# Kernel tuning notes

Measured on AMD Instinct MI355X. Metric: run time of the kernel, lower is better.

The kernel has to match this reference:

```python
import jax, jax.numpy as jnp
import numpy as np

CHAN = 24
INNER = 64
GROUPS = 8
M = 5
LAM = 1e-4
MAX_ITER = 25
BETA = 1.0
EPS = 1e-5
B, HH, WW = 128, 32, 32


def conv2d(x, w, b=None):
    # NCHW, OIHW, 3x3 SAME conv (padding = kernel//2)
    y = jax.lax.conv_general_dilated(x, w, (1, 1), 'SAME',
                                     dimension_numbers=('NCHW', 'OIHW', 'NCHW'))
    if b is not None:
        y = y + b[None, :, None, None]
    return y


def group_norm(x, g, b):
    bsz, c, h, w = x.shape
    xg = x.reshape(bsz, GROUPS, c // GROUPS, h, w)
    mu = xg.mean(axis=(2, 3, 4), keepdims=True)
    var = xg.var(axis=(2, 3, 4), keepdims=True)
    xn = ((xg - mu) / jnp.sqrt(var + EPS)).reshape(bsz, c, h, w)
    return xn * g[None, :, None, None] + b[None, :, None, None]


def batch_norm(x, g, b):
    # training-mode batch statistics over (N, H, W)
    mu = x.mean(axis=(0, 2, 3), keepdims=True)
    var = x.var(axis=(0, 2, 3), keepdims=True)
    return (x - mu) / jnp.sqrt(var + EPS) * g[None, :, None, None] + b[None, :, None, None]


def resnet_f(p, z, x):
    c1w, g1g, g1b, c2w, g2g, g2b, g3g, g3b = p
    y = group_norm(jax.nn.relu(conv2d(z, c1w)), g1g, g1b)
    return group_norm(jax.nn.relu(z + group_norm(x + conv2d(y, c2w), g2g, g2b)), g3g, g3b)


def anderson(f, x0):
    # Anderson acceleration, fixed MAX_ITER iterations (no host-sync tol break).
    bsz = x0.shape[0]
    d = x0.size // bsz
    X = jnp.zeros((bsz, M, d), x0.dtype)
    Fm = jnp.zeros((bsz, M, d), x0.dtype)
    f0 = f(x0).reshape(bsz, -1)
    X = X.at[:, 0].set(x0.reshape(bsz, -1))
    Fm = Fm.at[:, 0].set(f0)
    X = X.at[:, 1].set(f0)
    Fm = Fm.at[:, 1].set(f(f0.reshape(x0.shape)).reshape(bsz, -1))
    for k in range(2, MAX_ITER):
        n = min(k, M)
        G = Fm[:, :n] - X[:, :n]                       # [b, n, d]
        Hm = jnp.zeros((bsz, n + 1, n + 1), x0.dtype)
        Hm = Hm.at[:, 0, 1:].set(1.0).at[:, 1:, 0].set(1.0)
        Hm = Hm.at[:, 1:, 1:].set(jnp.einsum('bnd,bmd->bnm', G, G)
                                  + LAM * jnp.eye(n, dtype=x0.dtype)[None])
        yv = jnp.zeros((bsz, n + 1, 1), x0.dtype).at[:, 0, 0].set(1.0)
        alpha = jnp.linalg.solve(Hm, yv)[:, 1:, 0]     # [b, n]
        xnew = (BETA * jnp.einsum('bn,bnd->bd', alpha, Fm[:, :n])
                + (1.0 - BETA) * jnp.einsum('bn,bnd->bd', alpha, X[:, :n]))
        X = X.at[:, k % M].set(xnew)
        Fm = Fm.at[:, k % M].set(f(xnew.reshape(x0.shape)).reshape(bsz, -1))
    return X[:, (MAX_ITER - 1) % M].reshape(x0.shape)


def setup_inputs() -> dict:
    key = jax.random.key(0)
    ks = jax.random.split(key, 8)
    inp = {
        'x': jax.random.normal(ks[0], (B, 3, HH, WW), jnp.float32),
        'pre_conv_w': jax.random.normal(ks[1], (CHAN, 3, 3, 3), jnp.float32) * 0.1,
        'pre_conv_b': jnp.zeros((CHAN,), jnp.float32),
        'pre_bn_g': jnp.ones((CHAN,), jnp.float32),
        'pre_bn_b': jnp.zeros((CHAN,), jnp.float32),
        'f_conv1_w': jax.random.normal(ks[2], (INNER, CHAN, 3, 3), jnp.float32) * 0.01,
        'gn1_g': jnp.ones((INNER,), jnp.float32),
        'gn1_b': jnp.zeros((INNER,), jnp.float32),
        'f_conv2_w': jax.random.normal(ks[3], (CHAN, INNER, 3, 3), jnp.float32) * 0.01,
        'gn2_g': jnp.ones((CHAN,), jnp.float32),
        'gn2_b': jnp.zeros((CHAN,), jnp.float32),
        'gn3_g': jnp.ones((CHAN,), jnp.float32),
        'gn3_b': jnp.zeros((CHAN,), jnp.float32),
        'post_bn_g': jnp.ones((CHAN,), jnp.float32),
        'post_bn_b': jnp.zeros((CHAN,), jnp.float32),
        'fc_w': jax.random.normal(ks[4], (10, CHAN * 4 * 4), jnp.float32) * 0.05,
        'fc_b': jnp.zeros((10,), jnp.float32),
    }
    return inp


def reference(x, pre_conv_w, pre_conv_b, pre_bn_g, pre_bn_b,
              f_conv1_w, gn1_g, gn1_b, f_conv2_w, gn2_g, gn2_b, gn3_g, gn3_b,
              post_bn_g, post_bn_b, fc_w, fc_b):
    # pre: conv + BatchNorm
    xp = batch_norm(conv2d(x, pre_conv_w, pre_conv_b), pre_bn_g, pre_bn_b)
    p = (f_conv1_w, gn1_g, gn1_b, f_conv2_w, gn2_g, gn2_b, gn3_g, gn3_b)
    # DEQ fixed-point solve (eval path: train=False returns the fixed point)
    z_star = anderson(lambda z: resnet_f(p, z, xp), jnp.zeros_like(xp))
    z = resnet_f(p, z_star, xp)
    # post: relu -> BN -> avgpool(8,8) -> flatten -> linear
    h = batch_norm(jax.nn.relu(z), post_bn_g, post_bn_b)
    bsz, c, hh, ww = h.shape
    pooled = h.reshape(bsz, c, hh // 8, 8, ww // 8, 8).mean(axis=(3, 5))  # [B,C,4,4]
    return pooled.reshape(bsz, -1) @ fc_w.T + fc_b
```

## Files before the change

kernel.cpp:

```cpp
#include <hip/hip_runtime.h>
#include <hip/hip_bf16.h>

typedef __hip_bfloat16 bf16;
typedef unsigned short ushortT;
typedef __attribute__((ext_vector_type(8))) short short8;
typedef __attribute__((ext_vector_type(4))) float f32x4;

#define BB 128
#define CHAN 24
#define INNER 64
#define HW 1024
#define DD (CHAN*HW)

constexpr size_t cBD = (size_t)BB*DD;
constexpr size_t cYB = (size_t)BB*INNER*HW;

__device__ __attribute__((aligned(16))) ushortT g_xp[cBD];
__device__ __attribute__((aligned(16))) ushortT g_X[5*cBD];
__device__ __attribute__((aligned(16))) ushortT g_F[5*cBD];
__device__ __attribute__((aligned(16))) ushortT g_G[5*cBD];
__device__ __attribute__((aligned(16))) ushortT g_yb[cYB];
__device__ __attribute__((aligned(16))) ushortT g_tb[cBD];
__device__ __attribute__((aligned(16))) ushortT g_w1m[9*64*32];
__device__ __attribute__((aligned(16))) ushortT g_w2m[9*24*64];
__device__ __attribute__((aligned(16))) float g_stats2a[48];
__device__ __attribute__((aligned(16))) float g_stats2b[48];
__device__ __attribute__((aligned(16))) float g_gn1sum[BB*8*2];
__device__ __attribute__((aligned(16))) float g_gn2sum[BB*24*2];
__device__ __attribute__((aligned(16))) float g_gn3p[BB*4*16];
__device__ __attribute__((aligned(16))) float g_gramp[BB*4*5*5];
__device__ __attribute__((aligned(16))) float g_gram[BB*25];
__device__ __attribute__((aligned(16))) float g_pooled[BB*CHAN*16];
__device__ __attribute__((aligned(16))) float g_params[5120];
__device__ unsigned g_isbf16;

#define P_PCW 0
#define P_PCB 648
#define P_PBG 672
#define P_PBB 696
#define P_G1G 720
#define P_G1B 784
#define P_G2G 848
#define P_G2B 872
#define P_G3G 896
#define P_G3B 920
#define P_POG 944
#define P_POB 968
#define P_FCW 992
#define P_FCB 4832

__device__ __forceinline__ size_t aidx(int b, int icv, int pix){
  return (((size_t)b*3 + icv)*1024 + (size_t)pix)*8;
}
__device__ __forceinline__ float rdin(const void* p, int i){
// ... 50 lines not shown
                              g_params[P_POG+i]=rdin(pog,i);
                              g_params[P_POB+i]=rdin(pob,i); }
  for (int i=t;i<64;i+=256) { g_params[P_G1G+i]=rdin(g1g,i);
                              g_params[P_G1B+i]=rdin(g1b,i); }
  for (int i=t;i<3840;i+=256) g_params[P_FCW+i]=rdin(fcw,i);
  for (int i=t;i<10;i+=256)   g_params[P_FCB+i]=rdin(fcb,i);
  for (int i=t;i<48;i+=256) { g_stats2a[i]=0.f; g_stats2b[i]=0.f; }
}

__global__ void wtm_k(const void* w1, const void* w2){
  int t = blockIdx.x*256 + threadIdx.x;
  if (t < 9*64*32){
    int ic = t & 31, oc = (t>>5)&63, s9 = t>>11;
    float v = (ic<24) ? rdin(w1, (oc*24+ic)*9 + s9) : 0.f;
    g_w1m[t] = f2b(v);
  }
  int u = t - 9*64*32;
  if (u >= 0 && u < 9*24*64){
    int ic = u & 63; int rest = u >> 6; int oc = rest % 24; int s9 = rest / 24;
    g_w2m[u] = f2b(rdin(w2, (oc*64+ic)*9 + s9));
  }
}

__global__ void zeroX0_k(){
  size_t i = ((size_t)blockIdx.x*256 + threadIdx.x)*8;
  short8 z = {0,0,0,0,0,0,0,0};
  *(short8*)&g_X[i] = z;
  if (blockIdx.x < 8) g_gn1sum[blockIdx.x*256 + threadIdx.x] = 0.f;
}
__global__ void copyF0toX1_k(){
  size_t i = ((size_t)blockIdx.x*256 + threadIdx.x)*8;
  *(short8*)&g_X[cBD + i] = *(const short8*)&g_F[i];
  if (blockIdx.x < 8) g_gn1sum[blockIdx.x*256 + threadIdx.x] = 0.f;
}

__global__ void preconv_k(const void* __restrict__ x){
  int id = blockIdx.x*256 + threadIdx.x;
  int b = id >> 10, pix = id & 1023;
  int yy = pix >> 5, xx = pix & 31;
  float acc[24];
  #pragma unroll
  for (int oc=0;oc<24;oc++) acc[oc] = g_params[P_PCB+oc];
  for (int ic=0; ic<3; ic++)
    for (int ky=0; ky<3; ky++){
      int gy = yy+ky-1; if (gy<0||gy>=32) continue;
      for (int kx=0;kx<3;kx++){
        int gx = xx+kx-1; if (gx<0||gx>=32) continue;
        float v = rdin(x, ((b*3+ic)*32+gy)*32+gx);
        #pragma unroll
        for (int oc=0;oc<24;oc++)
          acc[oc] += v * g_params[P_PCW+(oc*3+ic)*9+ky*3+kx];
      }
    }
  st24c(g_tb, b, pix, acc);
}

template<bool RELU>
__global__ void bnstat2_k(int which){
// ... 22 lines not shown
    atomicAdd(&sRed[(icv*8+e)*2],   p0[e]);
    atomicAdd(&sRed[(icv*8+e)*2+1], p1[e]);
  }
  __syncthreads();
  if (t < 48) atomicAdd(&dst[t], sRed[t]);
}

__global__ void bn_apply_k(){
  int id = blockIdx.x*256+threadIdx.x;
  int b = id >> 10, pix = id & 1023;
  const float inv = 1.f/(BB*HW);
  float tv[24], ov[24];
  ld24c(g_tb, b, pix, tv);
  #pragma unroll
  for (int c=0;c<24;c++){
    float mean = g_stats2a[c*2]*inv;
    float var = fmaxf(g_stats2a[c*2+1]*inv - mean*mean, 0.f);
    float rstd = rsqrtf(var + 1e-5f);
    ov[c] = (tv[c]-mean)*rstd*g_params[P_PBG+c] + g_params[P_PBB+c];
  }
  st24c(g_xp, b, pix, ov);
}

__launch_bounds__(256, 2)
__global__ void conv1_k(int s){
  __shared__ ushortT sMem[29312];
  ushortT* sA = sMem;
  ushortT* sW = sMem + 10880;
  const int tid = threadIdx.x;
  const int lane = tid & 63, wv = tid >> 6;
  const int mLane = lane & 15, q = lane >> 4;
  const int b = blockIdx.x >> 2, yt = blockIdx.x & 3;
  const ushortT* __restrict__ Xs = g_X + (size_t)s*cBD;
  if (blockIdx.x < 24) g_gn2sum[blockIdx.x*256 + tid] = 0.f;
  for (int i = tid; i < 1360; i += 256){
    int icv = i & 3, apix = i >> 2;
    int yl = apix / 34, xl = apix - yl*34;
    int gy = yt*8 - 1 + yl, gx = xl - 1;
    short8 v = {0,0,0,0,0,0,0,0};
    if (gy >= 0 && gy < 32 && gx >= 0 && gx < 32 && icv < 3)
      v = *(const short8*)&Xs[aidx(b, icv, gy*32 + gx)];
    *(short8*)&sA[(size_t)(apix*4 + (icv ^ (apix&3)))*8] = v;
  }
  for (int i = tid; i < 2304; i += 256){
    int icv = i & 3, rest = i >> 2;
    int oc = rest & 63, s9 = rest >> 6;
    short8 v = *(const short8*)&g_w1m[(size_t)((s9*64 + oc)*32) + icv*8];
    *(short8*)&sW[(size_t)((s9*64+oc)*4 + (icv ^ (oc&3)))*8] = v;
  }
  __syncthreads();
  f32x4 acc[4][4];
  #pragma unroll
  for (int mt=0;mt<4;mt++)
    #pragma unroll
    for (int nt=0;nt<4;nt++) acc[mt][nt] = (f32x4){0.f,0.f,0.f,0.f};
  for (int s9=0; s9<9; s9++){
    int ky = s9/3, kx = s9 - ky*3;
    short8 bfr[4];
    #pragma unroll
    for (int nt=0;nt<4;nt++){
      int oc = nt*16 + mLane;
      bfr[nt] = *(const short8*)&sW[(size_t)((s9*64+oc)*4 + (q ^ (oc&3)))*8];
    }
    #pragma unroll
    for (int mt=0;mt<4;mt++){
      int g = wv*4+mt;
      int apix = ((g>>1) + ky)*34 + (g&1)*16 + mLane + kx;
      short8 afr = *(const short8*)&sA[(size_t)(apix*4 + (q ^ (apix&3)))*8];
      #pragma unroll
      for (int nt=0;nt<4;nt++)
        acc[mt][nt] = __builtin_amdgcn_mfma_f32_16x16x32_bf16(afr, bfr[nt], acc[mt][nt], 0,0,0);
    }
  }
  __syncthreads();
  ushortT* sOut = sMem;
  #pragma unroll
  for (int mt=0;mt<4;mt++){
    int g = wv*4+mt;
    #pragma unroll
    for (int nt=0;nt<4;nt++){
      int oc = nt*16 + mLane;
      #pragma unroll
      for (int r=0;r<4;r++){
        int pix = (g>>1)*32 + (g&1)*16 + q*4 + r;
        sOut[pix*64 + oc] = f2b(fmaxf(acc[mt][nt][r], 0.f));
      }
    }
  }
  __syncthreads();
  float s0=0.f, s1=0.f;
  size_t gbase = ((size_t)b*1024 + yt*256)*64;
  for (int c = tid; c < 2048; c += 256){
    short8 v = *(const short8*)&sOut[c*8];
    *(short8*)&g_yb[gbase + (size_t)c*8] = v;
    #pragma unroll
    for (int j=0;j<8;j++){ float f = b2f((ushortT)v[j]); s0 += f; s1 += f*f; }
  }
  s0 += __shfl_down(s0,32); s1 += __shfl_down(s1,32);
  s0 += __shfl_down(s0,16); s1 += __shfl_down(s1,16);
  s0 += __shfl_down(s0, 8); s1 += __shfl_down(s1, 8);
  if (lane < 8){
    atomicAdd(&g_gn1sum[(b*8+lane)*2],   s0);
    atomicAdd(&g_gn1sum[(b*8+lane)*2+1], s1);
  }
}

__launch_bounds__(256, 2)
__global__ void conv2_k(){
  __shared__ ushortT sMem[35584];
  __shared__ float sAff[128];
  ushortT* sA = sMem;
  ushortT* sW = sMem + 21760;
  const int tid = threadIdx.x;
  const int lane = tid & 63, wv = tid >> 6;
  const int mLane = lane & 15, q = lane >> 4;
  const int b = blockIdx.x >> 2, yt = blockIdx.x & 3;
  if (tid < 64){
    int c = tid, gr = c>>3;
    float S = g_gn1sum[(b*8+gr)*2], Q = g_gn1sum[(b*8+gr)*2+1];
    float mean = S*(1.f/8192.f);
    float var = fmaxf(Q*(1.f/8192.f) - mean*mean, 0.f);
    float rstd = rsqrtf(var + 1e-5f);
    float sc = rstd*g_params[P_G1G+c];
    sAff[c] = sc; sAff[64+c] = g_params[P_G1B+c] - mean*sc;
  }
  __syncthreads();
  for (int i = tid; i < 2720; i += 256){
    int icv = i & 7, apix = i >> 3;
    int yl = apix / 34, xl = apix - yl*34;
    int gy = yt*8 - 1 + yl, gx = xl - 1;
    short8 v = {0,0,0,0,0,0,0,0};
    if (gy >= 0 && gy < 32 && gx >= 0 && gx < 32){
      short8 raw = *(const short8*)&g_yb[((size_t)b*1024 + gy*32+gx)*64 + icv*8];
      #pragma unroll
      for (int j=0;j<8;j++){
        int c = icv*8+j;
        v[j] = (short)f2b(b2f((ushortT)raw[j])*sAff[c] + sAff[64+c]);
      }
    }
    *(short8*)&sA[(size_t)(apix*8 + (icv ^ (apix&7)))*8] = v;
  }
  for (int i = tid; i < 1728; i += 256){
    int icv = i & 7, rest = i >> 3;
    int oc = rest % 24, s9 = rest / 24;
    short8 v = *(const short8*)&g_w2m[(size_t)((s9*24+oc)*64) + icv*8];
    *(short8*)&sW[(size_t)((s9*24+oc)*8 + (icv ^ (oc&7)))*8] = v;
  }
  __syncthreads();
  f32x4 acc[4][2];
  #pragma unroll
  for (int mt=0;mt<4;mt++){ acc[mt][0]=(f32x4){0.f,0.f,0.f,0.f}; acc[mt][1]=(f32x4){0.f,0.f,0.f,0.f}; }
  const bool nt1ok = (mLane < 8);
  for (int s9=0; s9<9; s9++){
    int ky = s9/3, kx = s9 - ky*3;
    #pragma unroll
    for (int ks=0; ks<2; ks++){
      int ib = ks*4;
      short8 bfr[2];
      { int oc = mLane;
        bfr[0] = *(const short8*)&sW[(size_t)((s9*24+oc)*8 + ((ib+q) ^ (oc&7)))*8]; }
      if (nt1ok){
        int oc = 16 + mLane;
        bfr[1] = *(const short8*)&sW[(size_t)((s9*24+oc)*8 + ((ib+q) ^ (oc&7)))*8];
      } else bfr[1] = (short8){0,0,0,0,0,0,0,0};
      #pragma unroll
      for (int mt=0;mt<4;mt++){
        int g = wv*4+mt;
        int apix = ((g>>1) + ky)*34 + (g&1)*16 + mLane + kx;
        short8 afr = *(const short8*)&sA[(size_t)(apix*8 + ((ib+q) ^ (apix&7)))*8];
        acc[mt][0] = __builtin_amdgcn_mfma_f32_16x16x32_bf16(afr, bfr[0], acc[mt][0], 0,0,0);
        acc[mt][1] = __builtin_amdgcn_mfma_f32_16x16x32_bf16(afr, bfr[1], acc[mt][1], 0,0,0);
      }
    }
  }
  #pragma unroll
  for (int nt=0;nt<2;nt++){
    int oc = nt*16 + mLane;
    bool ok = (oc < 24);
    int icv = oc >> 3, e = oc & 7;
    float s0=0.f, s1=0.f;
    if (ok){
      #pragma unroll
      for (int mt=0;mt<4;mt++){
        int g = wv*4+mt;
        #pragma unroll
        for (int r=0;r<4;r++){
          int pix = (yt*8 + (g>>1))*32 + (g&1)*16 + q*4 + r;
          size_t o = aidx(b, icv, pix) + e;
          float v = acc[mt][nt][r] + b2f(g_xp[o]);
          g_tb[o] = f2b(v);
          s0 += v; s1 += v*v;
        }
      }
    }
    s0 += __shfl_down(s0,32); s1 += __shfl_down(s1,32);
    s0 += __shfl_down(s0,16); s1 += __shfl_down(s1,16);
    if (lane < 16 && ok){
      atomicAdd(&g_gn2sum[(b*24+oc)*2],   s0);
      atomicAdd(&g_gn2sum[(b*24+oc)*2+1], s1);
    }
  }
}

__launch_bounds__(256)
__global__ void fuse_a_k(int s){
  __shared__ float sM2[8], sR2[8], sSc2[24], sSb2[24];
  __shared__ float sRed[64];
  const int b = blockIdx.x>>2, seg = blockIdx.x&3;
  const int t = threadIdx.x;
  if (t < 8){
    float S = g_gn2sum[(b*24+t*3)*2]   + g_gn2sum[(b*24+t*3+1)*2]   + g_gn2sum[(b*24+t*3+2)*2];
    float Q = g_gn2sum[(b*24+t*3)*2+1] + g_gn2sum[(b*24+t*3+1)*2+1] + g_gn2sum[(b*24+t*3+2)*2+1];
    float m = S*(1.f/3072.f);
    sM2[t] = m;
    sR2[t] = rsqrtf(fmaxf(Q*(1.f/3072.f) - m*m, 0.f) + 1e-5f);
  }
  __syncthreads();
  if (t < 24){
    int g = t/3;
    float sc = sR2[g]*g_params[P_G2G+t];
    sSc2[t] = sc; sSb2[t] = g_params[P_G2B+t] - sM2[g]*sc;
  }
  __syncthreads();
  const int pix = seg*256 + t;
  float tv[24], xv[24];
  ld24c(g_tb, b, pix, tv);
  ld24c(g_X + (size_t)s*cBD, b, pix, xv);
  float p0[8], p1[8];
  #pragma unroll
  for (int g=0;g<8;g++){ p0[g]=0.f; p1[g]=0.f; }
  #pragma unroll
  for (int c=0;c<24;c++){
    int g = c/3;
    float v = fmaxf(xv[c] + tv[c]*sSc2[c] + sSb2[c], 0.f);
    p0[g] += v; p1[g] += v*v;
  }
  #pragma unroll
  for (int g=0;g<8;g++){
    for (int off=32;off>0;off>>=1){ p0[g]+=__shfl_down(p0[g],off,64); p1[g]+=__shfl_down(p1[g],off,64); }
  }
  int lane = t&63, wv = t>>6;
  if (lane==0){
    #pragma unroll
    for (int g=0;g<8;g++){ sRed[wv*16+g*2]=p0[g]; sRed[wv*16+g*2+1]=p1[g]; }
  }
  __syncthreads();
  if (t < 16){
    g_gn3p[(b*4+seg)*16 + t] = sRed[t]+sRed[16+t]+sRed[32+t]+sRed[48+t];
  }
}

__launch_bounds__(256)
__global__ void fuse_b_k(int s, int nv){
  __shared__ float sM2[8], sR2[8], sM3[8], sR3[8];
  __shared__ float sSc2[24], sSb2[24], sSc3[24], sSb3[24];
  __shared__ float sRedG[4][5];
  const int b = blockIdx.x>>2, seg = blockIdx.x&3;
  const int t = threadIdx.x;
  if (t < 8){
    float S = g_gn2sum[(b*24+t*3)*2]   + g_gn2sum[(b*24+t*3+1)*2]   + g_gn2sum[(b*24+t*3+2)*2];
    float Q = g_gn2sum[(b*24+t*3)*2+1] + g_gn2sum[(b*24+t*3+1)*2+1] + g_gn2sum[(b*24+t*3+2)*2+1];
    float m = S*(1.f/3072.f);
    sM2[t] = m;
    sR2[t] = rsqrtf(fmaxf(Q*(1.f/3072.f) - m*m, 0.f) + 1e-5f);
    float S3 = g_gn3p[(b*4+0)*16+t*2]   + g_gn3p[(b*4+1)*16+t*2]
             + g_gn3p[(b*4+2)*16+t*2]   + g_gn3p[(b*4+3)*16+t*2];
    float Q3 = g_gn3p[(b*4+0)*16+t*2+1] + g_gn3p[(b*4+1)*16+t*2+1]
             + g_gn3p[(b*4+2)*16+t*2+1] + g_gn3p[(b*4+3)*16+t*2+1];
    float m3 = S3*(1.f/3072.f);
    sM3[t] = m3;
    sR3[t] = rsqrtf(fmaxf(Q3*(1.f/3072.f) - m3*m3, 0.f) + 1e-5f);
  }
  __syncthreads();
  if (t < 24){
    int g = t/3;
    float sc2 = sR2[g]*g_params[P_G2G+t];
    sSc2[t] = sc2; sSb2[t] = g_params[P_G2B+t] - sM2[g]*sc2;
    float sc3 = sR3[g]*g_params[P_G3G+t];
    sSc3[t] = sc3; sSb3[t] = g_params[P_G3B+t] - sM3[g]*sc3;
  }
  __syncthreads();
  const int pix = seg*256 + t;
  float tv[24], xv[24], fv[24], gl[24];
  ld24c(g_tb, b, pix, tv);
  ld24c(g_X + (size_t)s*cBD, b, pix, xv);
  #pragma unroll
  for (int c=0;c<24;c++){
    float v = fmaxf(xv[c] + tv[c]*sSc2[c] + sSb2[c], 0.f);
    fv[c] = v*sSc3[c] + sSb3[c];
    float g = fv[c] - xv[c];
    gl[c] = b2f(f2b(g));
  }
  st24c(g_F + (size_t)s*cBD, b, pix, fv);
  st24c(g_G + (size_t)s*cBD, b, pix, gl);
  if (nv == 0) return;
  float part[5];
  #pragma unroll
  for (int j=0;j<5;j++) part[j]=0.f;
  #pragma unroll
  for (int j=0;j<5;j++){
    if (j>=nv) continue;
    float acc=0.f;
    if (j==s){
      #pragma unroll
      for (int c=0;c<24;c++) acc += gl[c]*gl[c];
    } else {
      float gv[24];
      ld24c(g_G + (size_t)j*cBD, b, pix, gv);
      #pragma unroll
      for (int c=0;c<24;c++) acc += gl[c]*gv[c];
    }
    part[j]=acc;
  }
  int lane = t&63, wv = t>>6;
  #pragma unroll
  for (int j=0;j<5;j++){
    float v = part[j];
    for (int off=32;off>0;off>>=1) v += __shfl_down(v,off,64);
    if (lane==0 && j<nv) sRedG[wv][j] = v;
  }
  __syncthreads();
  if (t < 5 && t < nv){
    float v = sRedG[0][t]+sRedG[1][t]+sRedG[2][t]+sRedG[3][t];
    g_gramp[((b*4+seg)*5 + s)*5 + t] = v;
  }
}

template<int N>
__device__ __forceinline__ void chol_alpha(const float Kf[5][5], float* alpha){
  double K[N][N];
  #pragma unroll
  for (int i=0;i<N;i++)
    #pragma unroll
    for (int j=0;j<N;j++)
      K[i][j] = (double)Kf[i][j] + (i==j ? 1e-4 : 0.0);
  #pragma unroll
  for (int c=0;c<N;c++){
    double d = K[c][c];
    #pragma unroll
    for (int k2=0;k2<c;k2++) d -= K[c][k2]*K[c][k2];
    d = sqrt(fmax(d, 1e-300));
    K[c][c] = d;
    double inv = 1.0/d;
    #pragma unroll
    for (int r=c+1;r<N;r++){
      double v = K[r][c];
      #pragma unroll
      for (int k2=0;k2<c;k2++) v -= K[r][k2]*K[c][k2];
      K[r][c] = v*inv;
    }
// ... 2 lines not shown
  #pragma unroll
  for (int i=0;i<N;i++){
    double v = 1.0;
    #pragma unroll
    for (int j=0;j<i;j++) v -= K[i][j]*y[j];
    y[i] = v / K[i][i];
  }
  double w[N];
  #pragma unroll
  for (int i=N-1;i>=0;i--){
    double v = y[i];
    #pragma unroll
    for (int j=i+1;j<N;j++) v -= K[j][i]*w[j];
    w[i] = v / K[i][i];
  }
  double sum = 0.0;
  #pragma unroll
  for (int i=0;i<N;i++) sum += w[i];
  double invs = 1.0/sum;
  #pragma unroll
  for (int i=0;i<N;i++) alpha[i] = (float)(w[i]*invs);
}

__global__ void xns_k(int s, int n, int rA, int nvA, int rB, int nvB){
  __shared__ float sAlpha[5];
  if (blockIdx.x < 8) g_gn1sum[blockIdx.x*256 + threadIdx.x] = 0.f;
  const int b = blockIdx.x >> 2, ch = blockIdx.x & 3;
  const int t = threadIdx.x;
  if (t == 0){
    float Kf[5][5];
    for (int i=0;i<n;i++)
      for (int j=0;j<n;j++) Kf[i][j] = g_gram[b*25 + i*5 + j];
    for (int j=0;j<nvA;j++){
      float v = g_gramp[((b*4+0)*5 + rA)*5 + j] + g_gramp[((b*4+1)*5 + rA)*5 + j]
              + g_gramp[((b*4+2)*5 + rA)*5 + j] + g_gramp[((b*4+3)*5 + rA)*5 + j];
      Kf[rA][j] = v; Kf[j][rA] = v;
    }
    if (rB >= 0){
      for (int j=0;j<nvB;j++){
        float v = g_gramp[((b*4+0)*5 + rB)*5 + j] + g_gramp[((b*4+1)*5 + rB)*5 + j]
                + g_gramp[((b*4+2)*5 + rB)*5 + j] + g_gramp[((b*4+3)*5 + rB)*5 + j];
        Kf[rB][j] = v; Kf[j][rB] = v;
      }
    }
    if (ch == 0){
      for (int j=0;j<nvA;j++){ g_gram[b*25+rA*5+j]=Kf[rA][j]; g_gram[b*25+j*5+rA]=Kf[rA][j]; }
      if (rB >= 0)
        for (int j=0;j<nvB;j++){ g_gram[b*25+rB*5+j]=Kf[rB][j]; g_gram[b*25+j*5+rB]=Kf[rB][j]; }
    }
    float al[5];
    if (n==2) chol_alpha<2>(Kf, al);
    else if (n==3) chol_alpha<3>(Kf, al);
    else if (n==4) chol_alpha<4>(Kf, al);
    else chol_alpha<5>(Kf, al);
    for (int j=0;j<n;j++) sAlpha[j] = al[j];
  }
  __syncthreads();
  float a[5];
  for (int j=0;j<n;j++) a[j] = sAlpha[j];
  const size_t base = (size_t)b*DD + (size_t)ch*6144;
  #pragma unroll
  for (int i=0;i<3;i++){
    size_t off = base + (size_t)i*2048 + (size_t)t*8;
    float acc[8];
    #pragma unroll
    for (int e=0;e<8;e++) acc[e]=0.f;
    for (int j=0;j<n;j++){
      short8 f = *(const short8*)&g_F[(size_t)j*cBD + off];
      float aj = a[j];
      #pragma unroll
      for (int e=0;e<8;e++) acc[e] += aj*b2f((ushortT)f[e]);
    }
    short8 o;
    #pragma unroll
    for (int e=0;e<8;e++) o[e] = (short)f2b(acc[e]);
    *(short8*)&g_X[(size_t)s*cBD + off] = o;
  }
}

__global__ void post_pool_k(){
  int i = blockIdx.x*256+threadIdx.x; if (i >= BB*CHAN*16) return;
  const ushortT* z = g_F + 4*cBD;
  int pw = i&3, ph=(i>>2)&3, c=(i>>4)%CHAN, bi=i/(CHAN*16);
  int icv = c>>3, e = c&7;
  float inv = 1.f/(BB*HW);
  float mean = g_stats2b[c*2]*inv;
  float var = fmaxf(g_stats2b[c*2+1]*inv - mean*mean, 0.f);
  float rstd = rsqrtf(var + 1e-5f);
  float gg=g_params[P_POG+c], bv=g_params[P_POB+c];
  float s=0.f;
  for (int dy=0;dy<8;dy++)
    for (int dx=0;dx<8;dx++){
      int pix = (ph*8+dy)*32 + pw*8+dx;
      float v = fmaxf(b2f(z[aidx(bi,icv,pix) + e]), 0.f);
      s += (v-mean)*rstd*gg + bv;
    }
  g_pooled[i] = s*(1.f/64.f);
}

// ... 10 lines not shown
                              void* d_out, int out_size, void* d_ws, size_t ws_size,
                              hipStream_t stream){
  const void* x   = d_in[0];
  const void* pcw = d_in[1];
  const void* pcb = d_in[2];
  const void* pbg = d_in[3];
  const void* pbb = d_in[4];
  const void* w1  = d_in[5];
  const void* g1g = d_in[6];
  const void* g1b = d_in[7];
  const void* w2  = d_in[8];
  const void* g2g = d_in[9];
  const void* g2b = d_in[10];
  const void* g3g = d_in[11];
  const void* g3b = d_in[12];
  const void* pog = d_in[13];
  const void* pob = d_in[14];
  const void* fcw = d_in[15];
  const void* fcb = d_in[16];
  (void)d_ws; (void)ws_size;

  const int gPix = (int)(BB*HW/256);

  auto feval = [&](int s, int nv){
    conv1_k<<<512,256,0,stream>>>(s);
    conv2_k<<<512,256,0,stream>>>();
    fuse_a_k<<<512,256,0,stream>>>(s);
    fuse_b_k<<<512,256,0,stream>>>(s, nv);
  };

  detect_k<<<1,64,0,stream>>>(g1g);
  cvt_params_k<<<1,256,0,stream>>>(pcw,pcb,pbg,pbb,g1g,g1b,g2g,g2b,g3g,g3b,pog,pob,fcw,fcb);
  wtm_k<<<126,256,0,stream>>>(w1, w2);

  preconv_k<<<gPix,256,0,stream>>>(x);
  bnstat2_k<false><<<512,192,0,stream>>>(0);
  bn_apply_k<<<gPix,256,0,stream>>>();

  zeroX0_k<<<1536,256,0,stream>>>();
  feval(0, 1);
  copyF0toX1_k<<<1536,256,0,stream>>>();
  feval(1, 2);

  for (int k=2;k<25;k++){
    int n = k<5 ? k : 5;
    int s = k%5;
    int nv = (k+1<5)?(k+1):5;
    if (k==2) xns_k<<<512,256,0,stream>>>(s, 2, 0, 1, 1, 2);
    else      xns_k<<<512,256,0,stream>>>(s, n, (k-1)%5, n, -1, 0);
    feval(s, (k<24) ? nv : 0);
  }

  bnstat2_k<true><<<512,192,0,stream>>>(1);
  post_pool_k<<<(BB*CHAN*16+255)/256,256,0,stream>>>();
  fc_k<<<(BB*10+255)/256,256,0,stream>>>(d_out);
}
```

Baseline: 1.592 ms.

## Fuse whole Anderson loop into one persistent per-sample kernel

Replaces the per-iteration launches of conv1, conv2, fuse_a, fuse_b and xns with a single anderson_k kernel that uses one 1024-thread block per batch sample and runs all 25 iterations inside it. Group-norm statistics, Gram rows and alpha are kept in shared memory instead of global atomics and partial buffers, and X shrinks to a single slot. This removes around a hundred kernel launches and the global statistics round-trips. In exchange only 128 blocks run across the GPU, and conv1/conv2 are processed one row tile at a time with far fewer waves per CU, so MFMA throughput and latency hiding may suffer.

```diff
diff --git a/kernel.cpp b/kernel.cpp
--- a/kernel.cpp
+++ b/kernel.cpp
@@ -16,7 +16,7 @@
 constexpr size_t cYB = (size_t)BB*INNER*HW;
 
 __device__ __attribute__((aligned(16))) ushortT g_xp[cBD];
-__device__ __attribute__((aligned(16))) ushortT g_X[5*cBD];
+__device__ __attribute__((aligned(16))) ushortT g_X[cBD];
 __device__ __attribute__((aligned(16))) ushortT g_F[5*cBD];
 __device__ __attribute__((aligned(16))) ushortT g_G[5*cBD];
 __device__ __attribute__((aligned(16))) ushortT g_yb[cYB];
@@ -25,11 +25,6 @@
 __device__ __attribute__((aligned(16))) ushortT g_w2m[9*24*64];
 __device__ __attribute__((aligned(16))) float g_stats2a[48];
 __device__ __attribute__((aligned(16))) float g_stats2b[48];
-__device__ __attribute__((aligned(16))) float g_gn1sum[BB*8*2];
-__device__ __attribute__((aligned(16))) float g_gn2sum[BB*24*2];
-__device__ __attribute__((aligned(16))) float g_gn3p[BB*4*16];
-__device__ __attribute__((aligned(16))) float g_gramp[BB*4*5*5];
-__device__ __attribute__((aligned(16))) float g_gram[BB*25];
 __device__ __attribute__((aligned(16))) float g_pooled[BB*CHAN*16];
 __device__ __attribute__((aligned(16))) float g_params[5120];
 __device__ unsigned g_isbf16;
@@ -126,18 +121,6 @@
   }
 }
 
-__global__ void zeroX0_k(){
-  size_t i = ((size_t)blockIdx.x*256 + threadIdx.x)*8;
-  short8 z = {0,0,0,0,0,0,0,0};
-  *(short8*)&g_X[i] = z;
-  if (blockIdx.x < 8) g_gn1sum[blockIdx.x*256 + threadIdx.x] = 0.f;
-}
-__global__ void copyF0toX1_k(){
-  size_t i = ((size_t)blockIdx.x*256 + threadIdx.x)*8;
-  *(short8*)&g_X[cBD + i] = *(const short8*)&g_F[i];
-  if (blockIdx.x < 8) g_gn1sum[blockIdx.x*256 + threadIdx.x] = 0.f;
-}
-
 __global__ void preconv_k(const void* __restrict__ x){
   int id = blockIdx.x*256 + threadIdx.x;
   int b = id >> 10, pix = id & 1023;
@@ -206,310 +189,6 @@
   st24c(g_xp, b, pix, ov);
 }
 
-__launch_bounds__(256, 2)
-__global__ void conv1_k(int s){
-  __shared__ ushortT sMem[29312];
-  ushortT* sA = sMem;
-  ushortT* sW = sMem + 10880;
-  const int tid = threadIdx.x;
-  const int lane = tid & 63, wv = tid >> 6;
-  const int mLane = lane & 15, q = lane >> 4;
-  const int b = blockIdx.x >> 2, yt = blockIdx.x & 3;
-  const ushortT* __restrict__ Xs = g_X + (size_t)s*cBD;
-  if (blockIdx.x < 24) g_gn2sum[blockIdx.x*256 + tid] = 0.f;
-  for (int i = tid; i < 1360; i += 256){
-    int icv = i & 3, apix = i >> 2;
-    int yl = apix / 34, xl = apix - yl*34;
-    int gy = yt*8 - 1 + yl, gx = xl - 1;
-    short8 v = {0,0,0,0,0,0,0,0};
-    if (gy >= 0 && gy < 32 && gx >= 0 && gx < 32 && icv < 3)
-      v = *(const short8*)&Xs[aidx(b, icv, gy*32 + gx)];
-    *(short8*)&sA[(size_t)(apix*4 + (icv ^ (apix&3)))*8] = v;
-  }
-  for (int i = tid; i < 2304; i += 256){
-    int icv = i & 3, rest = i >> 2;
-    int oc = rest & 63, s9 = rest >> 6;
-    short8 v = *(const short8*)&g_w1m[(size_t)((s9*64 + oc)*32) + icv*8];
-    *(short8*)&sW[(size_t)((s9*64+oc)*4 + (icv ^ (oc&3)))*8] = v;
-  }
-  __syncthreads();
-  f32x4 acc[4][4];
-  #pragma unroll
-  for (int mt=0;mt<4;mt++)
-    #pragma unroll
-    for (int nt=0;nt<4;nt++) acc[mt][nt] = (f32x4){0.f,0.f,0.f,0.f};
-  for (int s9=0; s9<9; s9++){
-    int ky = s9/3, kx = s9 - ky*3;
-    short8 bfr[4];
-    #pragma unroll
-    for (int nt=0;nt<4;nt++){
-      int oc = nt*16 + mLane;
-      bfr[nt] = *(const short8*)&sW[(size_t)((s9*64+oc)*4 + (q ^ (oc&3)))*8];
-    }
-    #pragma unroll
-    for (int mt=0;mt<4;mt++){
-      int g = wv*4+mt;
-      int apix = ((g>>1) + ky)*34 + (g&1)*16 + mLane + kx;
-      short8 afr = *(const short8*)&sA[(size_t)(apix*4 + (q ^ (apix&3)))*8];
-      #pragma unroll
-      for (int nt=0;nt<4;nt++)
-        acc[mt][nt] = __builtin_amdgcn_mfma_f32_16x16x32_bf16(afr, bfr[nt], acc[mt][nt], 0,0,0);
-    }
-  }
-  __syncthreads();
-  ushortT* sOut = sMem;
-  #pragma unroll
-  for (int mt=0;mt<4;mt++){
-    int g = wv*4+mt;
-    #pragma unroll
-    for (int nt=0;nt<4;nt++){
-      int oc = nt*16 + mLane;
-      #pragma unroll
-      for (int r=0;r<4;r++){
-        int pix = (g>>1)*32 + (g&1)*16 + q*4 + r;
-        sOut[pix*64 + oc] = f2b(fmaxf(acc[mt][nt][r], 0.f));
-      }
-    }
-  }
-  __syncthreads();
-  float s0=0.f, s1=0.f;
-  size_t gbase = ((size_t)b*1024 + yt*256)*64;
-  for (int c = tid; c < 2048; c += 256){
-    short8 v = *(const short8*)&sOut[c*8];
-    *(short8*)&g_yb[gbase + (size_t)c*8] = v;
-    #pragma unroll
-    for (int j=0;j<8;j++){ float f = b2f((ushortT)v[j]); s0 += f; s1 += f*f; }
-  }
-  s0 += __shfl_down(s0,32); s1 += __shfl_down(s1,32);
-  s0 += __shfl_down(s0,16); s1 += __shfl_down(s1,16);
-  s0 += __shfl_down(s0, 8); s1 += __shfl_down(s1, 8);
-  if (lane < 8){
-    atomicAdd(&g_gn1sum[(b*8+lane)*2],   s0);
-    atomicAdd(&g_gn1sum[(b*8+lane)*2+1], s1);
-  }
-}
-
-__launch_bounds__(256, 2)
-__global__ void conv2_k(){
-  __shared__ ushortT sMem[35584];
-  __shared__ float sAff[128];
-  ushortT* sA = sMem;
-  ushortT* sW = sMem + 21760;
-  const int tid = threadIdx.x;
-  const int lane = tid & 63, wv = tid >> 6;
-  const int mLane = lane & 15, q = lane >> 4;
-  const int b = blockIdx.x >> 2, yt = blockIdx.x & 3;
-  if (tid < 64){
-    int c = tid, gr = c>>3;
-    float S = g_gn1sum[(b*8+gr)*2], Q = g_gn1sum[(b*8+gr)*2+1];
-    float mean = S*(1.f/8192.f);
-    float var = fmaxf(Q*(1.f/8192.f) - mean*mean, 0.f);
-    float rstd = rsqrtf(var + 1e-5f);
-    float sc = rstd*g_params[P_G1G+c];
-    sAff[c] = sc; sAff[64+c] = g_params[P_G1B+c] - mean*sc;
-  }
-  __syncthreads();
-  for (int i = tid; i < 2720; i += 256){
-    int icv = i & 7, apix = i >> 3;
-    int yl = apix / 34, xl = apix - yl*34;
-    int gy = yt*8 - 1 + yl, gx = xl - 1;
-    short8 v = {0,0,0,0,0,0,0,0};
-    if (gy >= 0 && gy < 32 && gx >= 0 && gx < 32){
-      short8 raw = *(const short8*)&g_yb[((size_t)b*1024 + gy*32+gx)*64 + icv*8];
-      #pragma unroll
-      for (int j=0;j<8;j++){
-        int c = icv*8+j;
-        v[j] = (short)f2b(b2f((ushortT)raw[j])*sAff[c] + sAff[64+c]);
-      }
-    }
-    *(short8*)&sA[(size_t)(apix*8 + (icv ^ (apix&7)))*8] = v;
-  }
-  for (int i = tid; i < 1728; i += 256){
-    int icv = i & 7, rest = i >> 3;
-    int oc = rest % 24, s9 = rest / 24;
-    short8 v = *(const short8*)&g_w2m[(size_t)((s9*24+oc)*64) + icv*8];
-    *(short8*)&sW[(size_t)((s9*24+oc)*8 + (icv ^ (oc&7)))*8] = v;
-  }
-  __syncthreads();
-  f32x4 acc[4][2];
-  #pragma unroll
-  for (int mt=0;mt<4;mt++){ acc[mt][0]=(f32x4){0.f,0.f,0.f,0.f}; acc[mt][1]=(f32x4){0.f,0.f,0.f,0.f}; }
-  const bool nt1ok = (mLane < 8);
-  for (int s9=0; s9<9; s9++){
-    int ky = s9/3, kx = s9 - ky*3;
-    #pragma unroll
-    for (int ks=0; ks<2; ks++){
-      int ib = ks*4;
-      short8 bfr[2];
-      { int oc = mLane;
-        bfr[0] = *(const short8*)&sW[(size_t)((s9*24+oc)*8 + ((ib+q) ^ (oc&7)))*8]; }
-      if (nt1ok){
-        int oc = 16 + mLane;
-        bfr[1] = *(const short8*)&sW[(size_t)((s9*24+oc)*8 + ((ib+q) ^ (oc&7)))*8];
-      } else bfr[1] = (short8){0,0,0,0,0,0,0,0};
-      #pragma unroll
-      for (int mt=0;mt<4;mt++){
-        int g = wv*4+mt;
-        int apix = ((g>>1) + ky)*34 + (g&1)*16 + mLane + kx;
-        short8 afr = *(const short8*)&sA[(size_t)(apix*8 + ((ib+q) ^ (apix&7)))*8];
-        acc[mt][0] = __builtin_amdgcn_mfma_f32_16x16x32_bf16(afr, bfr[0], acc[mt][0], 0,0,0);
-        acc[mt][1] = __builtin_amdgcn_mfma_f32_16x16x32_bf16(afr, bfr[1], acc[mt][1], 0,0,0);
-      }
-    }
-  }
-  #pragma unroll
-  for (int nt=0;nt<2;nt++){
-    int oc = nt*16 + mLane;
-    bool ok = (oc < 24);
-    int icv = oc >> 3, e = oc & 7;
-    float s0=0.f, s1=0.f;
-    if (ok){
-      #pragma unroll
-      for (int mt=0;mt<4;mt++){
-        int g = wv*4+mt;
-        #pragma unroll
-        for (int r=0;r<4;r++){
-          int pix = (yt*8 + (g>>1))*32 + (g&1)*16 + q*4 + r;
-          size_t o = aidx(b, icv, pix) + e;
-          float v = acc[mt][nt][r] + b2f(g_xp[o]);
-          g_tb[o] = f2b(v);
-          s0 += v; s1 += v*v;
-        }
-      }
-    }
-    s0 += __shfl_down(s0,32); s1 += __shfl_down(s1,32);
-    s0 += __shfl_down(s0,16); s1 += __shfl_down(s1,16);
-    if (lane < 16 && ok){
-      atomicAdd(&g_gn2sum[(b*24+oc)*2],   s0);
-      atomicAdd(&g_gn2sum[(b*24+oc)*2+1], s1);
-    }
-  }
-}
-
-__launch_bounds__(256)
-__global__ void fuse_a_k(int s){
-  __shared__ float sM2[8], sR2[8], sSc2[24], sSb2[24];
-  __shared__ float sRed[64];
-  const int b = blockIdx.x>>2, seg = blockIdx.x&3;
-  const int t = threadIdx.x;
-  if (t < 8){
-    float S = g_gn2sum[(b*24+t*3)*2]   + g_gn2sum[(b*24+t*3+1)*2]   + g_gn2sum[(b*24+t*3+2)*2];
-    float Q = g_gn2sum[(b*24+t*3)*2+1] + g_gn2sum[(b*24+t*3+1)*2+1] + g_gn2sum[(b*24+t*3+2)*2+1];
-    float m = S*(1.f/3072.f);
-    sM2[t] = m;
-    sR2[t] = rsqrtf(fmaxf(Q*(1.f/3072.f) - m*m, 0.f) + 1e-5f);
-  }
-  __syncthreads();
-  if (t < 24){
-    int g = t/3;
-    float sc = sR2[g]*g_params[P_G2G+t];
-    sSc2[t] = sc; sSb2[t] = g_params[P_G2B+t] - sM2[g]*sc;
-  }
-  __syncthreads();
-  const int pix = seg*256 + t;
-  float tv[24], xv[24];
-  ld24c(g_tb, b, pix, tv);
-  ld24c(g_X + (size_t)s*cBD, b, pix, xv);
-  float p0[8], p1[8];
-  #pragma unroll
-  for (int g=0;g<8;g++){ p0[g]=0.f; p1[g]=0.f; }
-  #pragma unroll
-  for (int c=0;c<24;c++){
-    int g = c/3;
-    float v = fmaxf(xv[c] + tv[c]*sSc2[c] + sSb2[c], 0.f);
-    p0[g] += v; p1[g] += v*v;
-  }
-  #pragma unroll
-  for (int g=0;g<8;g++){
-    for (int off=32;off>0;off>>=1){ p0[g]+=__shfl_down(p0[g],off,64); p1[g]+=__shfl_down(p1[g],off,64); }
-  }
-  int lane = t&63, wv = t>>6;
-  if (lane==0){
-    #pragma unroll
-    for (int g=0;g<8;g++){ sRed[wv*16+g*2]=p0[g]; sRed[wv*16+g*2+1]=p1[g]; }
-  }
-  __syncthreads();
-  if (t < 16){
-    g_gn3p[(b*4+seg)*16 + t] = sRed[t]+sRed[16+t]+sRed[32+t]+sRed[48+t];
-  }
-}
-
-__launch_bounds__(256)
-__global__ void fuse_b_k(int s, int nv){
-  __shared__ float sM2[8], sR2[8], sM3[8], sR3[8];
-  __shared__ float sSc2[24], sSb2[24], sSc3[24], sSb3[24];
-  __shared__ float sRedG[4][5];
-  const int b = blockIdx.x>>2, seg = blockIdx.x&3;
-  const int t = threadIdx.x;
-  if (t < 8){
-    float S = g_gn2sum[(b*24+t*3)*2]   + g_gn2sum[(b*24+t*3+1)*2]   + g_gn2sum[(b*24+t*3+2)*2];
-    float Q = g_gn2sum[(b*24+t*3)*2+1] + g_gn2sum[(b*24+t*3+1)*2+1] + g_gn2sum[(b*24+t*3+2)*2+1];
-    float m = S*(1.f/3072.f);
-    sM2[t] = m;
-    sR2[t] = rsqrtf(fmaxf(Q*(1.f/3072.f) - m*m, 0.f) + 1e-5f);
-    float S3 = g_gn3p[(b*4+0)*16+t*2]   + g_gn3p[(b*4+1)*16+t*2]
-             + g_gn3p[(b*4+2)*16+t*2]   + g_gn3p[(b*4+3)*16+t*2];
-    float Q3 = g_gn3p[(b*4+0)*16+t*2+1] + g_gn3p[(b*4+1)*16+t*2+1]
-             + g_gn3p[(b*4+2)*16+t*2+1] + g_gn3p[(b*4+3)*16+t*2+1];
-    float m3 = S3*(1.f/3072.f);
-    sM3[t] = m3;
-    sR3[t] = rsqrtf(fmaxf(Q3*(1.f/3072.f) - m3*m3, 0.f) + 1e-5f);
-  }
-  __syncthreads();
-  if (t < 24){
-    int g = t/3;
-    float sc2 = sR2[g]*g_params[P_G2G+t];
-    sSc2[t] = sc2; sSb2[t] = g_params[P_G2B+t] - sM2[g]*sc2;
-    float sc3 = sR3[g]*g_params[P_G3G+t];
-    sSc3[t] = sc3; sSb3[t] = g_params[P_G3B+t] - sM3[g]*sc3;
-  }
-  __syncthreads();
-  const int pix = seg*256 + t;
-  float tv[24], xv[24], fv[24], gl[24];
-  ld24c(g_tb, b, pix, tv);
-  ld24c(g_X + (size_t)s*cBD, b, pix, xv);
-  #pragma unroll
-  for (int c=0;c<24;c++){
-    float v = fmaxf(xv[c] + tv[c]*sSc2[c] + sSb2[c], 0.f);
-    fv[c] = v*sSc3[c] + sSb3[c];
-    float g = fv[c] - xv[c];
-    gl[c] = b2f(f2b(g));
-  }
-  st24c(g_F + (size_t)s*cBD, b, pix, fv);
-  st24c(g_G + (size_t)s*cBD, b, pix, gl);
-  if (nv == 0) return;
-  float part[5];
-  #pragma unroll
-  for (int j=0;j<5;j++) part[j]=0.f;
-  #pragma unroll
-  for (int j=0;j<5;j++){
-    if (j>=nv) continue;
-    float acc=0.f;
-    if (j==s){
-      #pragma unroll
-      for (int c=0;c<24;c++) acc += gl[c]*gl[c];
-    } else {
-      float gv[24];
-      ld24c(g_G + (size_t)j*cBD, b, pix, gv);
-      #pragma unroll
-      for (int c=0;c<24;c++) acc += gl[c]*gv[c];
-    }
-    part[j]=acc;
-  }
-  int lane = t&63, wv = t>>6;
-  #pragma unroll
-  for (int j=0;j<5;j++){
-    float v = part[j];
-    for (int off=32;off>0;off>>=1) v += __shfl_down(v,off,64);
-    if (lane==0 && j<nv) sRedG[wv][j] = v;
-  }
-  __syncthreads();
-  if (t < 5 && t < nv){
-    float v = sRedG[0][t]+sRedG[1][t]+sRedG[2][t]+sRedG[3][t];
-    g_gramp[((b*4+seg)*5 + s)*5 + t] = v;
-  }
-}
-
 template<int N>
 __device__ __forceinline__ void chol_alpha(const float Kf[5][5], float* alpha){
   double K[N][N];
@@ -558,59 +237,288 @@
   for (int i=0;i<N;i++) alpha[i] = (float)(w[i]*invs);
 }
 
-__global__ void xns_k(int s, int n, int rA, int nvA, int rB, int nvB){
-  __shared__ float sAlpha[5];
-  if (blockIdx.x < 8) g_gn1sum[blockIdx.x*256 + threadIdx.x] = 0.f;
-  const int b = blockIdx.x >> 2, ch = blockIdx.x & 3;
-  const int t = threadIdx.x;
-  if (t == 0){
-    float Kf[5][5];
-    for (int i=0;i<n;i++)
-      for (int j=0;j<n;j++) Kf[i][j] = g_gram[b*25 + i*5 + j];
-    for (int j=0;j<nvA;j++){
-      float v = g_gramp[((b*4+0)*5 + rA)*5 + j] + g_gramp[((b*4+1)*5 + rA)*5 + j]
-              + g_gramp[((b*4+2)*5 + rA)*5 + j] + g_gramp[((b*4+3)*5 + rA)*5 + j];
-      Kf[rA][j] = v; Kf[j][rA] = v;
-    }
-    if (rB >= 0){
-      for (int j=0;j<nvB;j++){
-        float v = g_gramp[((b*4+0)*5 + rB)*5 + j] + g_gramp[((b*4+1)*5 + rB)*5 + j]
-                + g_gramp[((b*4+2)*5 + rB)*5 + j] + g_gramp[((b*4+3)*5 + rB)*5 + j];
-        Kf[rB][j] = v; Kf[j][rB] = v;
-      }
-    }
-    if (ch == 0){
-      for (int j=0;j<nvA;j++){ g_gram[b*25+rA*5+j]=Kf[rA][j]; g_gram[b*25+j*5+rA]=Kf[rA][j]; }
-      if (rB >= 0)
-        for (int j=0;j<nvB;j++){ g_gram[b*25+rB*5+j]=Kf[rB][j]; g_gram[b*25+j*5+rB]=Kf[rB][j]; }
-    }
-    float al[5];
-    if (n==2) chol_alpha<2>(Kf, al);
-    else if (n==3) chol_alpha<3>(Kf, al);
-    else if (n==4) chol_alpha<4>(Kf, al);
-    else chol_alpha<5>(Kf, al);
-    for (int j=0;j<n;j++) sAlpha[j] = al[j];
-  }
-  __syncthreads();
-  float a[5];
-  for (int j=0;j<n;j++) a[j] = sAlpha[j];
-  const size_t base = (size_t)b*DD + (size_t)ch*6144;
-  #pragma unroll
-  for (int i=0;i<3;i++){
-    size_t off = base + (size_t)i*2048 + (size_t)t*8;
-    float acc[8];
-    #pragma unroll
-    for (int e=0;e<8;e++) acc[e]=0.f;
-    for (int j=0;j<n;j++){
-      short8 f = *(const short8*)&g_F[(size_t)j*cBD + off];
-      float aj = a[j];
-      #pragma unroll
-      for (int e=0;e<8;e++) acc[e] += aj*b2f((ushortT)f[e]);
-    }
-    short8 o;
-    #pragma unroll
-    for (int e=0;e<8;e++) o[e] = (short)f2b(acc[e]);
-    *(short8*)&g_X[(size_t)s*cBD + off] = o;
+__launch_bounds__(1024, 1)
+__global__ void anderson_k(){
+  __shared__ ushortT sMem[29312];
+  __shared__ float sGram[25], sAlpha[5], sSum1[16], sSum2[48], sSum3[16], sGrow[5], sAff[128];
+  ushortT* sA = sMem;
+  ushortT* sW = sMem + 10880;
+  const int tid  = threadIdx.x;
+  const int b    = blockIdx.x;
+  const int lane = tid & 63, wv = tid >> 6;
+  const int mLane = lane & 15, q = lane >> 4;
+
+  #pragma unroll 1
+  for (int k = 0; k < 25; k++){
+    const int s  = (k < 2) ? k : (k % 5);
+    const int n  = (k < 5) ? k : 5;
+    const int nv = (k == 24) ? 0 : ((k+1 < 5) ? (k+1) : 5);
+
+    __syncthreads();
+    if (tid < 16) sSum1[tid] = 0.f;
+    else if (tid < 64) sSum2[tid-16] = 0.f;
+    else if (tid < 80) sSum3[tid-64] = 0.f;
+    else if (tid < 85) sGrow[tid-80] = 0.f;
+    if (tid == 0 && k >= 2){
+      float Kf[5][5];
+      for (int i=0;i<n;i++)
+        for (int j=0;j<n;j++) Kf[i][j] = sGram[i*5+j];
+      float al[5];
+      if (n==2) chol_alpha<2>(Kf, al);
+      else if (n==3) chol_alpha<3>(Kf, al);
+      else if (n==4) chol_alpha<4>(Kf, al);
+      else chol_alpha<5>(Kf, al);
+      for (int j=0;j<n;j++) sAlpha[j] = al[j];
+    }
+    __syncthreads();
+
+    {
+      const size_t xbase = (size_t)b*DD;
+      if (k == 0){
+        short8 z8 = {0,0,0,0,0,0,0,0};
+        for (int i=tid;i<3072;i+=1024) *(short8*)&g_X[xbase + (size_t)i*8] = z8;
+      } else if (k == 1){
+        for (int i=tid;i<3072;i+=1024)
+          *(short8*)&g_X[xbase + (size_t)i*8] = *(const short8*)&g_F[xbase + (size_t)i*8];
+      } else {
+        float a[5];
+        for (int j=0;j<n;j++) a[j] = sAlpha[j];
+        for (int i=tid;i<3072;i+=1024){
+          size_t off = xbase + (size_t)i*8;
+          float acc[8];
+          #pragma unroll
+          for (int e=0;e<8;e++) acc[e]=0.f;
+          for (int j=0;j<n;j++){
+            short8 f = *(const short8*)&g_F[(size_t)j*cBD + off];
+            float aj = a[j];
+            #pragma unroll
+            for (int e=0;e<8;e++) acc[e] += aj*b2f((ushortT)f[e]);
+          }
+          short8 o;
+          #pragma unroll
+          for (int e=0;e<8;e++) o[e] = (short)f2b(acc[e]);
+          *(short8*)&g_X[off] = o;
+        }
+      }
+    }
+    __syncthreads();
+
+    for (int i=tid;i<2304;i+=1024){
+      int icv = i & 3, rest = i >> 2;
+      int oc = rest & 63, s9 = rest >> 6;
+      short8 v = *(const short8*)&g_w1m[(size_t)((s9*64 + oc)*32) + icv*8];
+      *(short8*)&sW[(size_t)((s9*64+oc)*4 + (icv ^ (oc&3)))*8] = v;
+    }
+    for (int yt=0; yt<4; yt++){
+      for (int i=tid;i<1360;i+=1024){
+        int icv = i & 3, apix = i >> 2;
+        int yl = apix / 34, xl = apix - yl*34;
+        int gy = yt*8 - 1 + yl, gx = xl - 1;
+        short8 v = {0,0,0,0,0,0,0,0};
+        if (gy >= 0 && gy < 32 && gx >= 0 && gx < 32 && icv < 3)
+          v = *(const short8*)&g_X[aidx(b, icv, gy*32 + gx)];
+        *(short8*)&sA[(size_t)(apix*4 + (icv ^ (apix&3)))*8] = v;
+      }
+      __syncthreads();
+      f32x4 acc1[4];
+      #pragma unroll
+      for (int nt=0;nt<4;nt++) acc1[nt] = (f32x4){0.f,0.f,0.f,0.f};
+      for (int s9=0; s9<9; s9++){
+        int ky = s9/3, kx = s9 - ky*3;
+        short8 bfr[4];
+        #pragma unroll
+        for (int nt=0;nt<4;nt++){
+          int oc = nt*16 + mLane;
+          bfr[nt] = *(const short8*)&sW[(size_t)((s9*64+oc)*4 + (q ^ (oc&3)))*8];
+        }
+        int apix = ((wv>>1) + ky)*34 + (wv&1)*16 + mLane + kx;
+        short8 afr = *(const short8*)&sA[(size_t)(apix*4 + (q ^ (apix&3)))*8];
+        #pragma unroll
+        for (int nt=0;nt<4;nt++)
+          acc1[nt] = __builtin_amdgcn_mfma_f32_16x16x32_bf16(afr, bfr[nt], acc1[nt], 0,0,0);
+      }
+      #pragma unroll
+      for (int nt=0;nt<4;nt++){
+        int oc = nt*16 + mLane;
+        float s0 = 0.f, s1 = 0.f;
+        #pragma unroll
+        for (int r=0;r<4;r++){
+          int pixl = (wv>>1)*32 + (wv&1)*16 + q*4 + r;
+          float v = fmaxf(acc1[nt][r], 0.f);
+          s0 += v; s1 += v*v;
+          g_yb[((size_t)b*1024 + yt*256 + pixl)*64 + oc] = f2b(v);
+        }
+        s0 += __shfl_down(s0,32); s1 += __shfl_down(s1,32);
+        s0 += __shfl_down(s0,16); s1 += __shfl_down(s1,16);
+        s0 += __shfl_down(s0, 4); s1 += __shfl_down(s1, 4);
+        s0 += __shfl_down(s0, 2); s1 += __shfl_down(s1, 2);
+        s0 += __shfl_down(s0, 1); s1 += __shfl_down(s1, 1);
+        if (lane == 0){ atomicAdd(&sSum1[(nt*2+0)*2], s0); atomicAdd(&sSum1[(nt*2+0)*2+1], s1); }
+        if (lane == 8){ atomicAdd(&sSum1[(nt*2+1)*2], s0); atomicAdd(&sSum1[(nt*2+1)*2+1], s1); }
+      }
+      __syncthreads();
+    }
+
+    if (tid < 64){
+      int c = tid, gr = c>>3;
+      float S = sSum1[gr*2], Q = sSum1[gr*2+1];
+      float mean = S*(1.f/8192.f);
+      float var = fmaxf(Q*(1.f/8192.f) - mean*mean, 0.f);
+      float rstd = rsqrtf(var + 1e-5f);
+      float sc = rstd*g_params[P_G1G+c];
+      sAff[c] = sc; sAff[64+c] = g_params[P_G1B+c] - mean*sc;
+    }
+    for (int i=tid;i<1728;i+=1024){
+      int icv = i & 7, rest = i >> 3;
+      int oc = rest % 24, s9 = rest / 24;
+      short8 v = *(const short8*)&g_w2m[(size_t)((s9*24+oc)*64) + icv*8];
+      *(short8*)&sW[(size_t)((s9*24+oc)*8 + (icv ^ (oc&7)))*8] = v;
+    }
+    __syncthreads();
+    for (int yt=0; yt<4; yt++){
+      f32x4 acc2[2];
+      acc2[0] = (f32x4){0.f,0.f,0.f,0.f}; acc2[1] = (f32x4){0.f,0.f,0.f,0.f};
+      const bool nt1ok = (mLane < 8);
+      for (int h=0; h<2; h++){
+        for (int i=tid;i<1360;i+=1024){
+          int icv4 = i & 3, apix = i >> 2;
+          int yl = apix / 34, xl = apix - yl*34;
+          int gy = yt*8 - 1 + yl, gx = xl - 1;
+          short8 v = {0,0,0,0,0,0,0,0};
+          if (gy >= 0 && gy < 32 && gx >= 0 && gx < 32){
+            int icv = h*4 + icv4;
+            short8 raw = *(const short8*)&g_yb[((size_t)b*1024 + gy*32+gx)*64 + icv*8];
+            #pragma unroll
+            for (int j=0;j<8;j++){
+              int c = icv*8+j;
+              v[j] = (short)f2b(b2f((ushortT)raw[j])*sAff[c] + sAff[64+c]);
+            }
+          }
+          *(short8*)&sA[(size_t)(apix*4 + (icv4 ^ (apix&3)))*8] = v;
+        }
+        __syncthreads();
+        for (int s9=0; s9<9; s9++){
+          int ky = s9/3, kx = s9 - ky*3;
+          short8 bfr[2];
+          { int oc = mLane;
+            bfr[0] = *(const short8*)&sW[(size_t)((s9*24+oc)*8 + ((h*4+q) ^ (oc&7)))*8]; }
+          if (nt1ok){
+            int oc = 16 + mLane;
+            bfr[1] = *(const short8*)&sW[(size_t)((s9*24+oc)*8 + ((h*4+q) ^ (oc&7)))*8];
+          } else bfr[1] = (short8){0,0,0,0,0,0,0,0};
+          int apix = ((wv>>1) + ky)*34 + (wv&1)*16 + mLane + kx;
+          short8 afr = *(const short8*)&sA[(size_t)(apix*4 + (q ^ (apix&3)))*8];
+          acc2[0] = __builtin_amdgcn_mfma_f32_16x16x32_bf16(afr, bfr[0], acc2[0], 0,0,0);
+          acc2[1] = __builtin_amdgcn_mfma_f32_16x16x32_bf16(afr, bfr[1], acc2[1], 0,0,0);
+        }
+        __syncthreads();
+      }
+      #pragma unroll
+      for (int nt=0;nt<2;nt++){
+        int oc = nt*16 + mLane;
+        bool ok = (oc < 24);
+        int icv = oc >> 3, e = oc & 7;
+        float s0=0.f, s1=0.f;
+        if (ok){
+          #pragma unroll
+          for (int r=0;r<4;r++){
+            int pix = (yt*8 + (wv>>1))*32 + (wv&1)*16 + q*4 + r;
+            size_t o = aidx(b, icv, pix) + e;
+            float v = acc2[nt][r] + b2f(g_xp[o]);
+            g_tb[o] = f2b(v);
+            s0 += v; s1 += v*v;
+          }
+        }
+        s0 += __shfl_down(s0,32); s1 += __shfl_down(s1,32);
+        s0 += __shfl_down(s0,16); s1 += __shfl_down(s1,16);
+        if (lane < 16 && ok){
+          atomicAdd(&sSum2[oc*2],   s0);
+          atomicAdd(&sSum2[oc*2+1], s1);
+        }
+      }
+    }
+    __syncthreads();
+
+    if (tid < 24){
+      int g = tid/3;
+      float S = sSum2[(g*3)*2] + sSum2[(g*3+1)*2] + sSum2[(g*3+2)*2];
+      float Q = sSum2[(g*3)*2+1] + sSum2[(g*3+1)*2+1] + sSum2[(g*3+2)*2+1];
+      float m = S*(1.f/3072.f);
+      float rs = rsqrtf(fmaxf(Q*(1.f/3072.f) - m*m, 0.f) + 1e-5f);
+      float sc = rs*g_params[P_G2G+tid];
+      sAff[tid] = sc; sAff[24+tid] = g_params[P_G2B+tid] - m*sc;
+    }
+    __syncthreads();
+    {
+      float tv[24], xv[24];
+      ld24c(g_tb, b, tid, tv);
+      ld24c(g_X, b, tid, xv);
+      float p0[8], p1[8];
+      #pragma unroll
+      for (int g=0;g<8;g++){ p0[g]=0.f; p1[g]=0.f; }
+      #pragma unroll
+      for (int c=0;c<24;c++){
+        int g = c/3;
+        float v = fmaxf(xv[c] + tv[c]*sAff[c] + sAff[24+c], 0.f);
+        p0[g] += v; p1[g] += v*v;
+      }
+      #pragma unroll
+      for (int g=0;g<8;g++){
+        for (int off=32;off>0;off>>=1){ p0[g]+=__shfl_down(p0[g],off,64); p1[g]+=__shfl_down(p1[g],off,64); }
+      }
+      if (lane==0){
+        #pragma unroll
+        for (int g=0;g<8;g++){ atomicAdd(&sSum3[g*2], p0[g]); atomicAdd(&sSum3[g*2+1], p1[g]); }
+      }
+      __syncthreads();
+      if (tid < 24){
+        int g = tid/3;
+        float m3 = sSum3[g*2]*(1.f/3072.f);
+        float rs3 = rsqrtf(fmaxf(sSum3[g*2+1]*(1.f/3072.f) - m3*m3, 0.f) + 1e-5f);
+        float sc3 = rs3*g_params[P_G3G+tid];
+        sAff[48+tid] = sc3; sAff[72+tid] = g_params[P_G3B+tid] - m3*sc3;
+      }
+      __syncthreads();
+      float fv[24], gl[24];
+      #pragma unroll
+      for (int c=0;c<24;c++){
+        float v = fmaxf(xv[c] + tv[c]*sAff[c] + sAff[24+c], 0.f);
+        fv[c] = v*sAff[48+c] + sAff[72+c];
+        gl[c] = b2f(f2b(fv[c] - xv[c]));
+      }
+      st24c(g_F + (size_t)s*cBD, b, tid, fv);
+      st24c(g_G + (size_t)s*cBD, b, tid, gl);
+      if (nv > 0){
+        float part[5];
+        #pragma unroll
+        for (int j=0;j<5;j++) part[j]=0.f;
+        #pragma unroll
+        for (int j=0;j<5;j++){
+          if (j>=nv) continue;
+          float acc=0.f;
+          if (j==s){
+            #pragma unroll
+            for (int c=0;c<24;c++) acc += gl[c]*gl[c];
+          } else {
+            float gv[24];
+            ld24c(g_G + (size_t)j*cBD, b, tid, gv);
+            #pragma unroll
+            for (int c=0;c<24;c++) acc += gl[c]*gv[c];
+          }
+          part[j]=acc;
+        }
+        #pragma unroll
+        for (int j=0;j<5;j++){
+          float v = part[j];
+          for (int off=32;off>0;off>>=1) v += __shfl_down(v,off,64);
+          if (lane==0 && j<nv) atomicAdd(&sGrow[j], v);
+        }
+      }
+    }
+    __syncthreads();
+    if (tid == 0 && nv > 0){
+      for (int j=0;j<nv;j++){ sGram[s*5+j] = sGrow[j]; sGram[j*5+s] = sGrow[j]; }
+    }
   }
 }
 
@@ -667,13 +575,6 @@
 
   const int gPix = (int)(BB*HW/256);
 
-  auto feval = [&](int s, int nv){
-    conv1_k<<<512,256,0,stream>>>(s);
-    conv2_k<<<512,256,0,stream>>>();
-    fuse_a_k<<<512,256,0,stream>>>(s);
-    fuse_b_k<<<512,256,0,stream>>>(s, nv);
-  };
-
   detect_k<<<1,64,0,stream>>>(g1g);
   cvt_params_k<<<1,256,0,stream>>>(pcw,pcb,pbg,pbb,g1g,g1b,g2g,g2b,g3g,g3b,pog,pob,fcw,fcb);
   wtm_k<<<126,256,0,stream>>>(w1, w2);
@@ -682,19 +583,7 @@
   bnstat2_k<false><<<512,192,0,stream>>>(0);
   bn_apply_k<<<gPix,256,0,stream>>>();
 
-  zeroX0_k<<<1536,256,0,stream>>>();
-  feval(0, 1);
-  copyF0toX1_k<<<1536,256,0,stream>>>();
-  feval(1, 2);
-
-  for (int k=2;k<25;k++){
-    int n = k<5 ? k : 5;
-    int s = k%5;
-    int nv = (k+1<5)?(k+1):5;
-    if (k==2) xns_k<<<512,256,0,stream>>>(s, 2, 0, 1, 1, 2);
-    else      xns_k<<<512,256,0,stream>>>(s, n, (k-1)%5, n, -1, 0);
-    feval(s, (k<24) ? nv : 0);
-  }
+  anderson_k<<<128,1024,0,stream>>>();
 
   bnstat2_k<true><<<512,192,0,stream>>>(1);
   post_pool_k<<<(BB*CHAN*16+255)/256,256,0,stream>>>();
```

New measurement: 2.211 ms. 1.39x slower.
